# Kernel optimization log

Hardware: AMD Instinct MI355X
Metric: run time of the kernel (lower is better)

## Reference

```python
import jax, jax.numpy as jnp
import numpy as np

B, T, C, H, D, W = 4, 4096, 1024, 16, 64, 128  # batch, seq, n_embd, n_head, head_dim, window
NB = T // W  # number of query blocks
EPS = 1e-6


def _rms(x, w):
    # RMSNorm over last dim
    return x * jax.lax.rsqrt(jnp.mean(x * x, axis=-1, keepdims=True) + EPS) * w


def _rope(x, pos_ids):
    # MRoPE: pos_ids [T,3]; axis_id maps each freq to one of 3 axes
    inv_freq = 1.0 / (1e6 ** (jnp.arange(0, D, 2, dtype=jnp.float32) / D))  # [D/2]
    axis_id = jnp.arange(D // 2) % 3
    positions = pos_ids[:, axis_id].astype(jnp.float32)  # [T, D/2]
    freqs = positions * inv_freq  # [T, D/2]
    emb = jnp.concatenate([freqs, freqs], axis=-1)  # [T, D]
    cos = jnp.cos(emb)[None, None]  # [1,1,T,D]
    sin = jnp.sin(emb)[None, None]
    x1, x2 = x[..., : D // 2], x[..., D // 2 :]
    rot = jnp.concatenate([-x2, x1], axis=-1)
    return x * cos + rot * sin


def setup_inputs() -> dict:
    key = jax.random.key(0)
    ks = jax.random.split(key, 3)
    x = jax.random.normal(ks[0], (B, T, C), jnp.float32)
    pos = jnp.arange(T, dtype=jnp.int32)
    pos_ids = jnp.stack([pos, pos, pos], axis=-1)  # [T,3] text positions
    w_attn = jax.random.normal(ks[1], (C, C + 2 * D), jnp.float32) * 0.02
    w_proj = jax.random.normal(ks[2], (C, C), jnp.float32) * 0.02
    q_norm_w = jnp.ones((D,), jnp.float32)
    k_norm_w = jnp.ones((D,), jnp.float32)
    return {"x": x, "pos_ids": pos_ids, "w_attn": w_attn, "w_proj": w_proj,
            "q_norm_w": q_norm_w, "k_norm_w": k_norm_w}


def reference(x, pos_ids, w_attn, w_proj, q_norm_w, k_norm_w):
    # fused qkv projection (torch Linear without bias; weight stored [in,out])
    qkv = x @ w_attn  # [B,T,C+2D]
    q = qkv[..., :C].reshape(B, T, H, D).transpose(0, 2, 1, 3)  # [B,H,T,D]
    k = qkv[..., C : C + D][:, None]  # [B,1,T,D] single KV head (MQA)
    v = qkv[..., C + D :][:, None]  # [B,1,T,D]
    q = _rope(_rms(q, q_norm_w), pos_ids)
    k = _rope(_rms(k, k_norm_w), pos_ids)
    # sliding-window attention (q >= kv and q - kv <= W), computed in blocks of W
    qb = q.reshape(B, H, NB, W, D)
    kb = k.reshape(B, NB, W, D)
    vb = v.reshape(B, NB, W, D)
    kp = jnp.concatenate([jnp.zeros_like(kb[:, :1]), kb[:, :-1]], axis=1)  # prev k block
    vp = jnp.concatenate([jnp.zeros_like(vb[:, :1]), vb[:, :-1]], axis=1)
    kv_k = jnp.concatenate([kp, kb], axis=2)  # [B,NB,2W,D]
    kv_v = jnp.concatenate([vp, vb], axis=2)
    n = jnp.arange(NB)[:, None, None]
    qr = jnp.arange(W)[None, :, None]
    kr = jnp.arange(2 * W)[None, None, :]
    q_abs = n * W + qr
    kv_abs = (n - 1) * W + kr
    mask = (q_abs >= kv_abs) & (q_abs - kv_abs <= W) & (kv_abs >= 0)  # [NB,W,2W]
    scores = jnp.einsum("bhnqd,bnkd->bhnqk", qb, kv_k) / jnp.sqrt(jnp.float32(D))
    scores = jnp.where(mask[None, None], scores, -1e30)
    attn = jax.nn.softmax(scores, axis=-1)
    y = jnp.einsum("bhnqk,bnkd->bhnqd", attn, kv_v)  # [B,H,NB,W,D]
    y = y.reshape(B, H, T, D).transpose(0, 2, 1, 3).reshape(B, T, C)
    return y @ w_proj
```

## Files before the change

kernel.cpp:

```cpp
#include <hip/hip_runtime.h>


typedef __attribute__((ext_vector_type(8))) short short8;
typedef __attribute__((ext_vector_type(4))) float f32x4;
typedef __attribute__((ext_vector_type(16))) float f32x16;
typedef __attribute__((ext_vector_type(4))) unsigned uint4v;

#define DEV static __device__ __forceinline__

DEV unsigned short f2bf(float f) {
  unsigned u = __builtin_bit_cast(unsigned, f);
  u += 0x7fffu + ((u >> 16) & 1u);
  return (unsigned short)(u >> 16);
}
DEV float bf2f(unsigned short s) {
  unsigned u = ((unsigned)s) << 16;
  return __builtin_bit_cast(float, u);
}
DEV unsigned cvtpk(float a, float b) {
  unsigned r;
  asm("v_cvt_pk_bf16_f32 %0, %1, %2" : "=v"(r) : "v"(a), "v"(b));
  return r;
}

DEV f32x4 mfma16(short8 a, short8 b, f32x4 c) {
  return __builtin_amdgcn_mfma_f32_16x16x32_bf16(a, b, c, 0, 0, 0);
}
DEV f32x16 mfma32(short8 a, short8 b, f32x16 c) {
  return __builtin_amdgcn_mfma_f32_32x32x16_bf16(a, b, c, 0, 0, 0);
}

DEV void gload16(const void* g, void* l) {
  __builtin_amdgcn_global_load_lds(
      (const __attribute__((address_space(1))) unsigned int*)(unsigned long long)g,
      (__attribute__((address_space(3))) unsigned int*)(unsigned int)(unsigned long long)l,
      16, 0, 0);
}

#define BARRIER __builtin_amdgcn_s_barrier()
#define LGKM0  asm volatile("s_waitcnt lgkmcnt(0)" ::: "memory")
#define VMCNT4 asm volatile("s_waitcnt vmcnt(4)" ::: "memory")

__global__ __launch_bounds__(256) void k_cvt(const float* __restrict__ in,
                                             short* __restrict__ out, int n4) {
  int i = blockIdx.x * 256 + threadIdx.x;
  if (i >= n4) return;
  float4 v = ((const float4*)in)[i];
  short4 o;
  o.x = (short)f2bf(v.x); o.y = (short)f2bf(v.y);
  o.z = (short)f2bf(v.z); o.w = (short)f2bf(v.w);
  ((short4*)out)[i] = o;
}

__global__ __launch_bounds__(256) void k_tcvt(const float* __restrict__ W,
                                              short* __restrict__ Wt, int K, int N) {
  __shared__ float tl[32][33];
  int tx = threadIdx.x & 31, ty = threadIdx.x >> 5;
  int k0 = blockIdx.x * 32, n0 = blockIdx.y * 32;
#pragma unroll
  for (int i = 0; i < 4; ++i)
    tl[ty + i * 8][tx] = W[(size_t)(k0 + ty + i * 8) * N + n0 + tx];
  __syncthreads();
#pragma unroll
  for (int i = 0; i < 4; ++i)
    Wt[(size_t)(n0 + ty + i * 8) * K + k0 + tx] = (short)f2bf(tl[tx][ty + i * 8]);
}

__global__ __launch_bounds__(512, 2) void k_gemm256(const short* __restrict__ A,
                                                    const short* __restrict__ Bt,
                                                    void* __restrict__ Cout,
                                                    int M, int N, int K, int outBf16) {
  __shared__ short sm[65536];
  int nbn = N >> 8;
  int nwg = (M >> 8) * nbn;
  int bid = blockIdx.x;
  int swz = (bid & 7) * (nwg >> 3) + (bid >> 3);
  int bm = swz / nbn, bn = swz % nbn;
  int tid = threadIdx.x, wid = tid >> 6, lane = tid & 63;
  int wm = wid >> 2, wn = wid & 3;
  int lo = lane & 15, hi = lane >> 4;
  int NT = K >> 6;

  int r0 = tid >> 3, dc = tid & 7;
  int sc = dc ^ (r0 & 7);
  const short* aS0 = A  + (size_t)(bm * 256 + r0) * K + sc * 8;
  const short* bS0 = Bt + (size_t)(bn * 256 + r0) * K + sc * 8;
  size_t hstep = (size_t)128 * K;

  auto stage = [&](int jt, int mat, int h, int d) {
    const short* s = (mat ? bS0 : aS0) + (size_t)h * hstep + jt * 64;
    short* l = sm + d * 32768 + mat * 16384 + h * 8192;
    gload16(s,                     l + tid * 8);
    gload16(s + (size_t)64 * K,    l + 4096 + tid * 8);
  };

  int aRd[2];
#pragma unroll
  for (int kk = 0; kk < 2; ++kk)
    aRd[kk] = lo * 64 + (((kk << 2) | hi) ^ (lo & 7)) * 8;

  short8 Afr[8][2];
  short8 Bfr[2][2];
  f32x4 acc[8][4] = {};

  auto rdA = [&](int d, int m0) {
    int base = d * 32768 + wm * 8192;
#pragma unroll
    for (int m = 0; m < 4; ++m)
#pragma unroll
      for (int kk = 0; kk < 2; ++kk)
        Afr[m0 + m][kk] = *(const short8*)&sm[base + (m0 + m) * 1024 + aRd[kk]];
  };
  auto rdB = [&](int d, int n0) {
    int base = d * 32768 + 16384 + (wn >> 1) * 8192 + (wn & 1) * 4096;
#pragma unroll
    for (int nf = 0; nf < 2; ++nf)
#pragma unroll
      for (int kk = 0; kk < 2; ++kk)
        Bfr[nf][kk] = *(const short8*)&sm[base + (n0 + nf) * 1024 + aRd[kk]];
  };
  auto quad = [&](int m0, int n0) {
    __builtin_amdgcn_s_setprio(1);
#pragma unroll
    for (int m = 0; m < 4; ++m)
#pragma unroll
      for (int j = 0; j < 2; ++j)
#pragma unroll
        for (int kk = 0; kk < 2; ++kk)
          acc[m0 + m][n0 + j] = mfma16(Afr[m0 + m][kk], Bfr[j][kk], acc[m0 + m][n0 + j]);
    __builtin_amdgcn_s_setprio(0);
  };

  stage(0, 0, 0, 0); stage(0, 1, 0, 0); stage(0, 0, 1, 0); stage(0, 1, 1, 0);
  if (NT > 1) { stage(1, 0, 0, 1); stage(1, 1, 0, 1); }
  VMCNT4;
  BARRIER;

#pragma unroll 2
  for (int jt = 0; jt < NT; ++jt) {
    int d = jt & 1;
    rdA(d, 0); rdB(d, 0);
    if (jt + 1 < NT) stage(jt + 1, 0, 1, d ^ 1);
    BARRIER; LGKM0;
    quad(0, 0);
    BARRIER;
    rdA(d, 4);
    if (jt + 1 < NT) stage(jt + 1, 1, 1, d ^ 1);
    BARRIER; LGKM0;
    quad(4, 0);
    BARRIER;
    rdB(d, 2);
    if (jt + 2 < NT) stage(jt + 2, 0, 0, d);
    BARRIER; LGKM0;
    quad(0, 2);
    BARRIER;
    if (jt + 2 < NT) stage(jt + 2, 1, 0, d);
    VMCNT4;
    BARRIER;
    quad(4, 2);
    BARRIER;
  }

  int row0 = bm * 256 + wm * 128 + hi * 4;
  int col0 = bn * 256 + wn * 64 + lo;
  if (outBf16) {
    short* C = (short*)Cout;
#pragma unroll
    for (int m = 0; m < 8; ++m)
#pragma unroll
      for (int nf = 0; nf < 4; ++nf)
#pragma unroll
        for (int r = 0; r < 4; ++r)
          C[(size_t)(row0 + m * 16 + r) * N + col0 + nf * 16] = (short)f2bf(acc[m][nf][r]);
  } else {
    float* C = (float*)Cout;
#pragma unroll
    for (int m = 0; m < 8; ++m)
#pragma unroll
      for (int nf = 0; nf < 4; ++nf)
#pragma unroll
        for (int r = 0; r < 4; ++r)
          C[(size_t)(row0 + m * 16 + r) * N + col0 + nf * 16] = acc[m][nf][r];
  }
}

__global__ __launch_bounds__(256) void k_qk(const short* __restrict__ qkvb,
                                            const int* __restrict__ pos,
                                            const float* __restrict__ qw,
                                            const float* __restrict__ kw,
                                            short* __restrict__ qb,
                                            short* __restrict__ kb) {
  int bt = blockIdx.x * 4 + (threadIdx.x >> 6);
  int t = bt & 4095, b = bt >> 12;
  int d = threadIdx.x & 63;
  int j = d & 31;
  float invf = __expf((float)j * (-13.815510558f / 32.f));
  float sn, cs;
  sincosf((float)pos[t * 3 + (j % 3)] * invf, &sn, &cs);
  const short* base = qkvb + (size_t)bt * 1280;
  float wq = qw[d], wk = kw[d];

  auto rowproc = [&](float x, float w) -> float {
    float ss = x * x;
    ss += __shfl_xor(ss, 1);  ss += __shfl_xor(ss, 2);  ss += __shfl_xor(ss, 4);
    ss += __shfl_xor(ss, 8);  ss += __shfl_xor(ss, 16); ss += __shfl_xor(ss, 32);
    float xn = x * rsqrtf(ss * 0.015625f + 1e-6f) * w;
    float pr = __shfl_xor(xn, 32);
    return (d < 32) ? xn * cs - pr * sn : xn * cs + pr * sn;
  };
  {
    float x = bf2f((unsigned short)base[1024 + d]);
    kb[(size_t)bt * 64 + d] = (short)f2bf(rowproc(x, wk));
  }
#pragma unroll 4
  for (int hh = 0; hh < 16; ++hh) {
    float x = bf2f((unsigned short)base[hh * 64 + d]);
    qb[((size_t)((b * 16 + hh) * 4096 + t)) * 64 + d] = (short)f2bf(rowproc(x, wq));
  }
}

__global__ __launch_bounds__(256) void k_vt(const short* __restrict__ qkvb,
                                            short* __restrict__ vtg) {
  __shared__ short ts[64][72];
  int t0 = blockIdx.x * 64;
  int b = t0 >> 12, tl0 = t0 & 4095;
  int row = threadIdx.x >> 2, c4 = threadIdx.x & 3;
  const short* src = qkvb + (size_t)(t0 + row) * 1280 + 1088 + c4 * 16;
  *(short8*)&ts[row][c4 * 16]     = *(const short8*)src;
  *(short8*)&ts[row][c4 * 16 + 8] = *(const short8*)(src + 8);
  __syncthreads();
  short8 o0, o1;
#pragma unroll
  for (int jj = 0; jj < 8; ++jj) {
    o0[jj] = ts[c4 * 16 + jj][row];
    o1[jj] = ts[c4 * 16 + 8 + jj][row];
  }
  short* dst = vtg + (size_t)(b * 64 + row) * 4096 + tl0 + c4 * 16;
  *(short8*)dst = o0;
  *(short8*)(dst + 8) = o1;
}

__global__ __launch_bounds__(256, 4) void k_attn(const short* __restrict__ qb,
                                                 const short* __restrict__ kb,
                                                 const short* __restrict__ vtg,
                                                 short* __restrict__ y) {
  __shared__ __align__(16) char smem[33792];
  short* ks  = (short*)smem;
  short* vts = (short*)(smem + 16384);
  int bid = blockIdx.x;
  int swz = (bid & 7) * 256 + (bid >> 3);
  int h = swz & 15, n = (swz >> 4) & 31, b = swz >> 9;
  int tid = threadIdx.x, wid = tid >> 6, lane = tid & 63;
  int lo = lane & 31, hi = lane >> 5;

  const short* qrow = qb + (size_t)((b * 16 + h) * 4096 + n * 128 + wid * 32 + lo) * 64;
  short8 aq[4];
#pragma unroll
  for (int s = 0; s < 4; ++s) aq[s] = *(const short8*)(qrow + s * 16 + hi * 8);

  f32x16 O0 = {}, O1 = {};
  float mrun = -1e30f, lrun = 0.f;
  int qr = wid * 32 + lo;
  const float SC = 0.125f * 1.4426950408889634f;

  for (int hf = (n == 0) ? 1 : 0; hf < 2; ++hf) {
    int tg = (n - 1 + hf) * 128;
#pragma unroll
    for (int p = 0; p < 4; ++p) {
      int idx = p * 256 + tid;
      int r = idx >> 3, dc = idx & 7;
      gload16(kb + (size_t)(b * 4096 + tg + r) * 64 + ((dc ^ (r & 7)) << 3),
              ks + idx * 8);
    }
#pragma unroll
    for (int p = 0; p < 4; ++p) {
      int idx = p * 256 + tid;
      int dd = idx >> 4, s = idx & 15;
      gload16(vtg + (size_t)(b * 64 + dd) * 4096 + tg + ((s ^ (dd & 7)) << 3),
              vts + idx * 8);
    }
    __syncthreads();

#pragma unroll
    for (int mt = 0; mt < 4; ++mt) {
      f32x16 S = {};
      int r = mt * 32 + lo;
#pragma unroll
      for (int kst = 0; kst < 4; ++kst) {
        short8 kf = *(const short8*)&ks[r * 64 + ((((kst << 1) | hi) ^ (r & 7)) << 3)];
        S = mfma32(kf, aq[kst], S);
      }
#pragma unroll
      for (int rr = 0; rr < 16; ++rr) {
        int kg = hf * 128 + mt * 32 + (rr & 3) + ((rr >> 2) << 3) + (hi << 2);
        S[rr] = (kg >= qr && kg <= qr + 128) ? S[rr] * SC : -30000.f;
      }
      float pmax = S[0];
#pragma unroll
      for (int rr = 1; rr < 16; ++rr) pmax = fmaxf(pmax, S[rr]);
      pmax = fmaxf(pmax, __shfl_xor(pmax, 32));
      if (!__all(pmax - mrun <= 8.f)) {
        float mn = fmaxf(mrun, pmax);
        float al = exp2f(mrun - mn);
        lrun *= al; mrun = mn;
#pragma unroll
        for (int rr = 0; rr < 16; ++rr) { O0[rr] *= al; O1[rr] *= al; }
      }
      float ls = 0.f;
#pragma unroll
      for (int rr = 0; rr < 16; ++rr) { S[rr] = exp2f(S[rr] - mrun); ls += S[rr]; }
      ls += __shfl_xor(ls, 32);
      lrun += ls;
#pragma unroll
      for (int h2 = 0; h2 < 2; ++h2) {
        int b0 = h2 * 8;
        unsigned pk0 = cvtpk(S[b0 + 0], S[b0 + 1]);
        unsigned pk1 = cvtpk(S[b0 + 2], S[b0 + 3]);
        unsigned pk2 = cvtpk(S[b0 + 4], S[b0 + 5]);
        unsigned pk3 = cvtpk(S[b0 + 6], S[b0 + 7]);
        asm("v_permlane32_swap_b32 %0, %1" : "+v"(pk0), "+v"(pk2));
        asm("v_permlane32_swap_b32 %0, %1" : "+v"(pk1), "+v"(pk3));
        uint4v uw; uw.x = pk0; uw.y = pk1; uw.z = pk2; uw.w = pk3;
        short8 pb = __builtin_bit_cast(short8, uw);
        int kc = mt * 4 + h2 * 2 + hi;
        short8 vb0 = *(const short8*)&vts[lo * 128 + ((kc ^ (lo & 7)) << 3)];
        short8 vb1 = *(const short8*)&vts[(32 + lo) * 128 + ((kc ^ (lo & 7)) << 3)];
        O0 = mfma32(vb0, pb, O0);
        O1 = mfma32(vb1, pb, O1);
      }
    }
    __syncthreads();
  }

  float inv = 1.f / lrun;
  float* ot = (float*)smem + wid * 2112;
#pragma unroll
  for (int r = 0; r < 16; ++r) {
    int d0 = (r & 3) + ((r >> 2) << 3) + (hi << 2);
    ot[d0 * 33 + lo]        = O0[r] * inv;
    ot[(d0 + 32) * 33 + lo] = O1[r] * inv;
  }
  __syncthreads();
  int tok = lane >> 3, dc = lane & 7;
#pragma unroll
  for (int g = 0; g < 4; ++g) {
    int q = g * 8 + tok;
    short8 o8;
#pragma unroll
    for (int jj = 0; jj < 8; ++jj)
      o8[jj] = (short)f2bf(ot[(dc * 8 + jj) * 33 + q]);
    *(short8*)&y[(size_t)(b * 4096 + n * 128 + wid * 32 + q) * 1024 + h * 64 + dc * 8] = o8;
  }
}

extern "C" void kernel_launch(void* const* d_in, const int* in_sizes, int n_in,
                              void* d_out, int out_size, void* d_ws, size_t ws_size,
                              hipStream_t stream) {
  const float* x      = (const float*)d_in[0];
  const int*   pos    = (const int*)d_in[1];
  const float* w_attn = (const float*)d_in[2];
  const float* w_proj = (const float*)d_in[3];
  const float* qw     = (const float*)d_in[4];
  const float* kw     = (const float*)d_in[5];

  char* ws = (char*)d_ws;
  short* xb   = (short*)ws;
  short* wabt = (short*)(ws + 33554432);
  short* wpbt = (short*)(ws + 36175872);
  short* qkvb = (short*)(ws + 38273024);
  short* qb2  = (short*)(ws + 80216064);
  short* kb2  = (short*)(ws + 113770496);
  short* vtg  = (short*)(ws + 115867648);
  short* ybuf = xb;

  hipLaunchKernelGGL(k_cvt, dim3(16384), dim3(256), 0, stream, x, xb, 4194304);
  hipLaunchKernelGGL(k_tcvt, dim3(32, 36), dim3(256), 0, stream, w_attn, wabt, 1024, 1152);
  hipLaunchKernelGGL(k_tcvt, dim3(32, 32), dim3(256), 0, stream, w_proj, wpbt, 1024, 1024);
  hipLaunchKernelGGL(k_gemm256, dim3(320), dim3(512), 0, stream, xb, wabt, (void*)qkvb,
                     16384, 1280, 1024, 1);
  hipLaunchKernelGGL(k_qk, dim3(4096), dim3(256), 0, stream, qkvb, pos, qw, kw, qb2, kb2);
  hipLaunchKernelGGL(k_vt, dim3(256), dim3(256), 0, stream, qkvb, vtg);
  hipLaunchKernelGGL(k_attn, dim3(2048), dim3(256), 0, stream, qb2, kb2, vtg, ybuf);
  hipLaunchKernelGGL(k_gemm256, dim3(256), dim3(512), 0, stream, ybuf, wpbt, d_out,
                     16384, 1024, 1024, 0);
}
```

Measured before the change: 190.9 us.

## Fuse QK RMSNorm+RoPE and V transpose into QKV GEMM epilogue

The QKV projection GEMM now applies RMSNorm and RoPE to the Q and K tiles in its epilogue, transposes the V tile through shared memory, and writes the head-major q, k and transposed v buffers directly. This removes the intermediate qkv buffer round-trip through global memory and the separate k_qk and k_vt launches. A small k_trig kernel precomputes the cos/sin tables so the epilogue only does table lookups. The cost is a heavier GEMM epilogue with extra register pressure and shared-memory staging, plus columns 1152-1279 (the padded tile region) are simply dropped.

```diff
diff --git a/kernel.cpp b/kernel.cpp
--- a/kernel.cpp
+++ b/kernel.cpp
@@ -66,10 +66,26 @@
     Wt[(size_t)(n0 + ty + i * 8) * K + k0 + tx] = (short)f2bf(tl[tx][ty + i * 8]);
 }
 
-__global__ __launch_bounds__(512, 2) void k_gemm256(const short* __restrict__ A,
-                                                    const short* __restrict__ Bt,
-                                                    void* __restrict__ Cout,
-                                                    int M, int N, int K, int outBf16) {
+__global__ __launch_bounds__(256) void k_trig(const int* __restrict__ pos,
+                                              float* __restrict__ ct,
+                                              float* __restrict__ st) {
+  int idx = blockIdx.x * 256 + threadIdx.x;
+  int t = idx >> 5, j = idx & 31;
+  float invf = __expf((float)j * (-13.815510558f / 32.f));
+  float p = (float)pos[t * 3 + (j % 3)];
+  float s, c;
+  sincosf(p * invf, &s, &c);
+  ct[idx] = c;
+  st[idx] = s;
+}
+
+__global__ __launch_bounds__(512, 2) void k_gemm256(
+    const short* __restrict__ A, const short* __restrict__ Bt,
+    void* __restrict__ Cout, int M, int N, int K, int outBf16,
+    const float* __restrict__ ct, const float* __restrict__ st,
+    const float* __restrict__ qw, const float* __restrict__ kw,
+    short* __restrict__ qb2, short* __restrict__ kb2, short* __restrict__ vtg,
+    int mode) {
   __shared__ short sm[65536];
   int nbn = N >> 8;
   int nwg = (M >> 8) * nbn;
@@ -161,6 +177,76 @@
     BARRIER;
   }
 
+  if (mode == 1) {
+    int tg0 = (bm * 256 + wm * 128) & 4095;
+    int bb  = (bm * 256) >> 12;
+    bool isQ = bn < 4, isK = (bn == 4 && wn == 0), isV = (bn == 4 && wn == 1);
+    short* smw = sm + wid * 8192;
+    if (isQ || isK) {
+      const float* nw = isQ ? qw : kw;
+      float w0 = nw[lo], w1 = nw[16 + lo], w2 = nw[32 + lo], w3 = nw[48 + lo];
+#pragma unroll
+      for (int m = 0; m < 8; ++m)
+#pragma unroll
+        for (int r = 0; r < 4; ++r) {
+          float x0 = acc[m][0][r], x1 = acc[m][1][r];
+          float x2 = acc[m][2][r], x3 = acc[m][3][r];
+          float ss = x0 * x0 + x1 * x1 + x2 * x2 + x3 * x3;
+          ss += __shfl_xor(ss, 1); ss += __shfl_xor(ss, 2);
+          ss += __shfl_xor(ss, 4); ss += __shfl_xor(ss, 8);
+          float rn = rsqrtf(ss * 0.015625f + 1e-6f);
+          x0 *= rn * w0; x1 *= rn * w1; x2 *= rn * w2; x3 *= rn * w3;
+          int tp = m * 16 + hi * 4 + r;
+          int tloc = tg0 + tp;
+          float c0 = ct[tloc * 32 + lo],      s0 = st[tloc * 32 + lo];
+          float c1 = ct[tloc * 32 + 16 + lo], s1 = st[tloc * 32 + 16 + lo];
+          float o0 = x0 * c0 - x2 * s0;
+          float o1 = x1 * c1 - x3 * s1;
+          float o2 = x2 * c0 + x0 * s0;
+          float o3 = x3 * c1 + x1 * s1;
+          smw[tp * 64 + lo]      = (short)f2bf(o0);
+          smw[tp * 64 + 16 + lo] = (short)f2bf(o1);
+          smw[tp * 64 + 32 + lo] = (short)f2bf(o2);
+          smw[tp * 64 + 48 + lo] = (short)f2bf(o3);
+        }
+    } else if (isV) {
+#pragma unroll
+      for (int m = 0; m < 8; ++m)
+#pragma unroll
+        for (int nf = 0; nf < 4; ++nf)
+#pragma unroll
+          for (int r = 0; r < 4; ++r)
+            smw[(nf * 16 + lo) * 128 + m * 16 + hi * 4 + r] =
+                (short)f2bf(acc[m][nf][r]);
+    }
+    __syncthreads();
+    if (isQ) {
+      int hh = bn * 4 + wn;
+      short* dst = qb2 + (size_t)(bb * 16 + hh) * 4096 * 64;
+#pragma unroll
+      for (int i = 0; i < 16; ++i) {
+        int c = i * 64 + lane, tp = c >> 3, d2 = c & 7;
+        *(short8*)&dst[(size_t)(tg0 + tp) * 64 + d2 * 8] =
+            *(const short8*)&smw[tp * 64 + d2 * 8];
+      }
+    } else if (isK) {
+#pragma unroll
+      for (int i = 0; i < 16; ++i) {
+        int c = i * 64 + lane, tp = c >> 3, d2 = c & 7;
+        *(short8*)&kb2[((size_t)bb * 4096 + tg0 + tp) * 64 + d2 * 8] =
+            *(const short8*)&smw[tp * 64 + d2 * 8];
+      }
+    } else if (isV) {
+#pragma unroll
+      for (int i = 0; i < 16; ++i) {
+        int c = i * 64 + lane, dd = c >> 4, tc = c & 15;
+        *(short8*)&vtg[((size_t)(bb * 64 + dd)) * 4096 + tg0 + tc * 8] =
+            *(const short8*)&smw[dd * 128 + tc * 8];
+      }
+    }
+    return;
+  }
+
   int row0 = bm * 256 + wm * 128 + hi * 4;
   int col0 = bn * 256 + wn * 64 + lo;
   if (outBf16) {
@@ -182,62 +268,6 @@
         for (int r = 0; r < 4; ++r)
           C[(size_t)(row0 + m * 16 + r) * N + col0 + nf * 16] = acc[m][nf][r];
   }
-}
-
-__global__ __launch_bounds__(256) void k_qk(const short* __restrict__ qkvb,
-                                            const int* __restrict__ pos,
-                                            const float* __restrict__ qw,
-                                            const float* __restrict__ kw,
-                                            short* __restrict__ qb,
-                                            short* __restrict__ kb) {
-  int bt = blockIdx.x * 4 + (threadIdx.x >> 6);
-  int t = bt & 4095, b = bt >> 12;
-  int d = threadIdx.x & 63;
-  int j = d & 31;
-  float invf = __expf((float)j * (-13.815510558f / 32.f));
-  float sn, cs;
-  sincosf((float)pos[t * 3 + (j % 3)] * invf, &sn, &cs);
-  const short* base = qkvb + (size_t)bt * 1280;
-  float wq = qw[d], wk = kw[d];
-
-  auto rowproc = [&](float x, float w) -> float {
-    float ss = x * x;
-    ss += __shfl_xor(ss, 1);  ss += __shfl_xor(ss, 2);  ss += __shfl_xor(ss, 4);
-    ss += __shfl_xor(ss, 8);  ss += __shfl_xor(ss, 16); ss += __shfl_xor(ss, 32);
-    float xn = x * rsqrtf(ss * 0.015625f + 1e-6f) * w;
-    float pr = __shfl_xor(xn, 32);
-    return (d < 32) ? xn * cs - pr * sn : xn * cs + pr * sn;
-  };
-  {
-    float x = bf2f((unsigned short)base[1024 + d]);
-    kb[(size_t)bt * 64 + d] = (short)f2bf(rowproc(x, wk));
-  }
-#pragma unroll 4
-  for (int hh = 0; hh < 16; ++hh) {
-    float x = bf2f((unsigned short)base[hh * 64 + d]);
-    qb[((size_t)((b * 16 + hh) * 4096 + t)) * 64 + d] = (short)f2bf(rowproc(x, wq));
-  }
-}
-
-__global__ __launch_bounds__(256) void k_vt(const short* __restrict__ qkvb,
-                                            short* __restrict__ vtg) {
-  __shared__ short ts[64][72];
-  int t0 = blockIdx.x * 64;
-  int b = t0 >> 12, tl0 = t0 & 4095;
-  int row = threadIdx.x >> 2, c4 = threadIdx.x & 3;
-  const short* src = qkvb + (size_t)(t0 + row) * 1280 + 1088 + c4 * 16;
-  *(short8*)&ts[row][c4 * 16]     = *(const short8*)src;
-  *(short8*)&ts[row][c4 * 16 + 8] = *(const short8*)(src + 8);
-  __syncthreads();
-  short8 o0, o1;
-#pragma unroll
-  for (int jj = 0; jj < 8; ++jj) {
-    o0[jj] = ts[c4 * 16 + jj][row];
-    o1[jj] = ts[c4 * 16 + 8 + jj][row];
-  }
-  short* dst = vtg + (size_t)(b * 64 + row) * 4096 + tl0 + c4 * 16;
-  *(short8*)dst = o0;
-  *(short8*)(dst + 8) = o1;
 }
 
 __global__ __launch_bounds__(256, 4) void k_attn(const short* __restrict__ qb,
@@ -367,20 +397,24 @@
   short* xb   = (short*)ws;
   short* wabt = (short*)(ws + 33554432);
   short* wpbt = (short*)(ws + 36175872);
-  short* qkvb = (short*)(ws + 38273024);
-  short* qb2  = (short*)(ws + 80216064);
-  short* kb2  = (short*)(ws + 113770496);
-  short* vtg  = (short*)(ws + 115867648);
+  short* qb2  = (short*)(ws + 38273024);
+  short* kb2  = (short*)(ws + 71827456);
+  short* vtg  = (short*)(ws + 73924608);
+  float* ctab = (float*)(ws + 76021760);
+  float* stab = (float*)(ws + 76546048);
   short* ybuf = xb;
 
   hipLaunchKernelGGL(k_cvt, dim3(16384), dim3(256), 0, stream, x, xb, 4194304);
   hipLaunchKernelGGL(k_tcvt, dim3(32, 36), dim3(256), 0, stream, w_attn, wabt, 1024, 1152);
   hipLaunchKernelGGL(k_tcvt, dim3(32, 32), dim3(256), 0, stream, w_proj, wpbt, 1024, 1024);
-  hipLaunchKernelGGL(k_gemm256, dim3(320), dim3(512), 0, stream, xb, wabt, (void*)qkvb,
-                     16384, 1280, 1024, 1);
-  hipLaunchKernelGGL(k_qk, dim3(4096), dim3(256), 0, stream, qkvb, pos, qw, kw, qb2, kb2);
-  hipLaunchKernelGGL(k_vt, dim3(256), dim3(256), 0, stream, qkvb, vtg);
+  hipLaunchKernelGGL(k_trig, dim3(512), dim3(256), 0, stream, pos, ctab, stab);
+  hipLaunchKernelGGL(k_gemm256, dim3(320), dim3(512), 0, stream, xb, wabt,
+                     (void*)nullptr, 16384, 1280, 1024, 1,
+                     ctab, stab, qw, kw, qb2, kb2, vtg, 1);
   hipLaunchKernelGGL(k_attn, dim3(2048), dim3(256), 0, stream, qb2, kb2, vtg, ybuf);
   hipLaunchKernelGGL(k_gemm256, dim3(256), dim3(512), 0, stream, ybuf, wpbt, d_out,
-                     16384, 1024, 1024, 0);
-}
+                     16384, 1024, 1024, 0,
+                     (const float*)nullptr, (const float*)nullptr,
+                     (const float*)nullptr, (const float*)nullptr,
+                     (short*)nullptr, (short*)nullptr, (short*)nullptr, 0);
+}
```

Measured after the change: 175.7 us. -8.0%, faster.
